# Optimization experiments

Hardware: AMD Instinct MI355X
Metric: run time of the kernel (lower is better)

## Reference

```python
import jax, jax.numpy as jnp
import numpy as np

B, M, C, S, SD, K, H = 32, 448, 384, 512, 128, 8, 8
DH = C // H
EPS = 1e-5
NEG_SLOPE = 0.2


def setup_inputs() -> dict:
    key = jax.random.key(0)
    ks = iter(jax.random.split(key, 32))
    nrm = lambda shape, scale=0.05: (jax.random.normal(next(ks), shape, jnp.float32) * scale)
    inp = {
        'q': jax.random.normal(next(ks), (B, M, C), jnp.float32),
        'coarse': jax.random.normal(next(ks), (B, M, 3), jnp.float32),
        'skeleton': jax.random.normal(next(ks), (B, S, 3), jnp.float32),
        # GraphConv 1: 3 -> 64 (root weight, rel/neighbor weight, bias)
        'gc1_wroot': nrm((3, 64), 0.3), 'gc1_wrel': nrm((3, 64), 0.3), 'gc1_b': jnp.zeros((64,), jnp.float32),
        # GraphConv 2: 64 -> SD
        'gc2_wroot': nrm((64, SD), 0.1), 'gc2_wrel': nrm((64, SD), 0.1), 'gc2_b': jnp.zeros((SD,), jnp.float32),
        # skeleton_projection: SD -> C
        'proj_w': nrm((SD, C), 0.08), 'proj_b': jnp.zeros((C,), jnp.float32),
        # MultiheadAttention (torch layout: in_proj (3C, C), out_proj (C, C))
        'attn_in_w': nrm((3 * C, C), 0.05), 'attn_in_b': jnp.zeros((3 * C,), jnp.float32),
        'attn_out_w': nrm((C, C), 0.05), 'attn_out_b': jnp.zeros((C,), jnp.float32),
        # increase_dim: Conv1d(C,1024,1) + BN(1024) + LeakyReLU + Conv1d(1024,1024,1)
        'inc1_w': nrm((1024, C), 0.05), 'inc1_b': jnp.zeros((1024,), jnp.float32),
        'bn_g': jnp.ones((1024,), jnp.float32), 'bn_b': jnp.zeros((1024,), jnp.float32),
        'bn_m': jnp.zeros((1024,), jnp.float32), 'bn_v': jnp.ones((1024,), jnp.float32),
        'inc2_w': nrm((1024, 1024), 0.03), 'inc2_b': jnp.zeros((1024,), jnp.float32),
        # reduce_map: Linear(C + 1024 + 3, C)
        'red_w': nrm((1024 + C + 3, C), 0.03), 'red_b': jnp.zeros((C,), jnp.float32),
    }
    return inp


def _knn_idx(pts):
    # pts: [B,S,3]; per-batch kNN (self excluded), matching knn_graph(k=K, batch=...)
    d2 = jnp.sum((pts[:, :, None, :] - pts[:, None, :, :]) ** 2, axis=-1)  # [B,S,S]
    d2 = d2 + jnp.eye(S, dtype=pts.dtype)[None] * 1e10                       # mask self
    _, idx = jax.lax.top_k(-d2, K)                                           # [B,S,K]
    return idx


def _graph_conv(x, idx, wroot, wrel, b):
    # GraphConv (PyG, aggr='add'): out_i = x_i Wroot + (sum_{j in N(i)} x_j) Wrel + b
    nb = jax.vmap(lambda f, i: f[i])(x, idx)   # [B,S,K,F]
    agg = nb.sum(axis=2)                       # [B,S,F]
    return x @ wroot + agg @ wrel + b


def reference(q, coarse, skeleton, gc1_wroot, gc1_wrel, gc1_b, gc2_wroot, gc2_wrel, gc2_b,
              proj_w, proj_b, attn_in_w, attn_in_b, attn_out_w, attn_out_b,
              inc1_w, inc1_b, bn_g, bn_b, bn_m, bn_v, inc2_w, inc2_b, red_w, red_b):
    # --- skeleton branch: knn graph + 2-layer GraphConv + max-pool + projection ---
    idx = _knn_idx(skeleton)
    h = _graph_conv(skeleton, idx, gc1_wroot, gc1_wrel, gc1_b)
    h = jax.nn.relu(h)
    h = _graph_conv(h, idx, gc2_wroot, gc2_wrel, gc2_b)        # [B,S,SD]
    proxy = jnp.max(h, axis=1)                                  # [B,SD]
    proxy = proxy @ proj_w + proj_b                             # [B,C]
    kv = jnp.broadcast_to(proxy[:, None, :], (B, M, C))         # expanded proxies

    # --- cross attention (torch nn.MultiheadAttention math) ---
    wq, wk, wv = attn_in_w[:C], attn_in_w[C:2 * C], attn_in_w[2 * C:]
    bq, bk, bv = attn_in_b[:C], attn_in_b[C:2 * C], attn_in_b[2 * C:]
    qh = (q @ wq.T + bq).reshape(B, M, H, DH)
    kh = (kv @ wk.T + bk).reshape(B, M, H, DH)
    vh = (kv @ wv.T + bv).reshape(B, M, H, DH)
    scores = jnp.einsum('bmhd,bnhd->bhmn', qh, kh) / jnp.sqrt(jnp.float32(DH))
    attn = jax.nn.softmax(scores, axis=-1)
    ctx = jnp.einsum('bhmn,bnhd->bmhd', attn, vh).reshape(B, M, C)
    q = ctx @ attn_out_w.T + attn_out_b                         # fused features [B,M,C]

    # --- increase_dim (1x1 conv == matmul) + BN(eval) + LeakyReLU + 1x1 conv ---
    g = jnp.einsum('bmc,oc->bmo', q, inc1_w) + inc1_b           # [B,M,1024]
    g = bn_g * (g - bn_m) * jax.lax.rsqrt(bn_v + EPS) + bn_b
    g = jnp.where(g >= 0, g, NEG_SLOPE * g)
    g = jnp.einsum('bmc,oc->bmo', g, inc2_w) + inc2_b
    global_feature = jnp.max(g, axis=1)                         # [B,1024]

    # --- concat + reduce_map ---
    rebuild = jnp.concatenate([jnp.broadcast_to(global_feature[:, None, :], (B, M, 1024)), q, coarse], axis=-1)
    out = rebuild @ red_w + red_b                               # [B,M,C]
    return out
```

## Files before the change

kernel.cpp:

```cpp
#include <hip/hip_runtime.h>

#define NB 32
#define MM 448
#define CC 384
#define SS 512
#define KNN 8

#define WS_IDX   0u
#define WS_H1    524288u
#define WS_PMAX  (WS_H1 + 4194304u)
#define WS_Q     (WS_PMAX + 262144u)
#define WS_Y     (WS_Q + 49152u)
#define WS_G2    (WS_Y + 131072u)
#define WS_BASEP (WS_G2 + 131072u)
#define WS_PP    WS_H1
#define WS_KV    WS_IDX
#define WS_VV    (WS_IDX + 49152u)

__device__ __forceinline__ float wave_sum(float v) {
#pragma unroll
  for (int m = 1; m < 64; m <<= 1) v += __shfl_xor(v, m, 64);
  return v;
}

__global__ __launch_bounds__(256) void k_knn_gc1(
    const float* __restrict__ skel,
    const float* __restrict__ w1root, const float* __restrict__ w1rel,
    const float* __restrict__ b1,
    int* __restrict__ idx_ws, float* __restrict__ h1_ws)
{
  int b   = blockIdx.x >> 7;
  int grp = blockIdx.x & 127;
  __shared__ __align__(16) float4 sk[SS];
  const float* sb = skel + b * SS * 3;
  for (int t = threadIdx.x; t < SS; t += 256)
    sk[t] = make_float4(sb[t*3+0], sb[t*3+1], sb[t*3+2], 0.f);
  __syncthreads();

  int wave = threadIdx.x >> 6, lane = threadIdx.x & 63;
  int i = grp * 4 + wave;
  float4 pi = sk[i];

  float bd[KNN];
#pragma unroll
  for (int t = 0; t < KNN; t++) {
    int j = lane + (t << 6);
    float4 p = sk[j];
    float d2;
    {
#pragma clang fp contract(off)
      float dx = pi.x - p.x, dy = pi.y - p.y, dz = pi.z - p.z;
      d2 = (dx*dx + dy*dy) + dz*dz;
    }
    bd[t] = (j == i) ? 3e38f : d2;
  }

  int win[KNN];
  int* idx_base = idx_ws + (size_t)(b*SS + i) * KNN;
#pragma unroll
  for (int t = 0; t < KNN; t++) {
    float bestd = bd[0]; int bests = 0;
#pragma unroll
    for (int s = 1; s < KNN; s++)
      if (bd[s] < bestd) { bestd = bd[s]; bests = s; }
    int bestj = lane + (bests << 6);
#pragma unroll
    for (int m = 1; m < 64; m <<= 1) {
      float od = __shfl_xor(bestd, m, 64);
      int   oj = __shfl_xor(bestj, m, 64);
      if (od < bestd || (od == bestd && oj < bestj)) { bestd = od; bestj = oj; }
    }
    win[t] = bestj;
    if (lane == t) idx_base[t] = bestj;
    if ((bestj & 63) == lane) {
      int sl = bestj >> 6;
#pragma unroll
      for (int s = 0; s < KNN; s++) if (s == sl) bd[s] = 3e38f;
    }
  }

  float a0 = 0.f, a1 = 0.f, a2 = 0.f;
#pragma unroll
  for (int t = 0; t < KNN; t++) {
    float4 n = sk[win[t]];
    a0 += n.x; a1 += n.y; a2 += n.z;
  }

  int c = lane;
  float h = b1[c] + pi.x*w1root[c] + pi.y*w1root[64+c] + pi.z*w1root[128+c]
                  + a0*w1rel[c]   + a1*w1rel[64+c]   + a2*w1rel[128+c];
  h = fmaxf(h, 0.f);
  h1_ws[(size_t)(b*SS + i) * 64 + lane] = h;
}

__global__ __launch_bounds__(256) void k_gc2_max(
    const float* __restrict__ h1_ws, const int* __restrict__ idx_ws,
    const float* __restrict__ w2root, const float* __restrict__ w2rel,
    const float* __restrict__ b2, float* __restrict__ pmax)
{
  int b = blockIdx.x >> 4, chunk = blockIdx.x & 15;
  int r0 = chunk * 32;
  __shared__ __align__(16) float X[32*129];
  __shared__ __align__(16) float Wt[32*128];
  __shared__ float mred[8*128];
  __shared__ int nbs[32*KNN];

  const float* h1b = h1_ws + (size_t)b * SS * 64;
  nbs[threadIdx.x] = idx_ws[(b*SS + r0)*KNN + threadIdx.x];
#pragma unroll
  for (int p = 0; p < 8; p++) {
    int idx = threadIdx.x + 256*p;
    int r = idx >> 6, k = idx & 63;
    X[r*129 + k] = h1b[(r0 + r)*64 + k];
  }
  __syncthreads();
#pragma unroll
  for (int p = 0; p < 8; p++) {
    int idx = threadIdx.x + 256*p;
    int r = idx >> 6, k = idx & 63;
    const int* nb = nbs + r*KNN;
    float s = 0.f;
#pragma unroll
    for (int j = 0; j < KNN; j++) s += h1b[nb[j]*64 + k];
    X[r*129 + 64 + k] = s;
  }

  int rg = threadIdx.x >> 5, cg = threadIdx.x & 31;
  float acc[4][4];
#pragma unroll
  for (int r = 0; r < 4; r++)
#pragma unroll
    for (int u = 0; u < 4; u++) acc[r][u] = 0.f;

  const float* wsrc[4] = { w2root, w2root + 32*128, w2rel, w2rel + 32*128 };
#pragma unroll 1
  for (int ch = 0; ch < 4; ch++) {
    __syncthreads();
    const float* ws = wsrc[ch];
#pragma unroll
    for (int p = 0; p < 16; p++) {
      int idx = threadIdx.x + 256*p;
      Wt[idx] = ws[idx];
    }
    __syncthreads();
    int kb = ch * 32;
    const float* xr0 = X + (rg*4+0)*129 + kb;
    const float* xr1 = X + (rg*4+1)*129 + kb;
    const float* xr2 = X + (rg*4+2)*129 + kb;
    const float* xr3 = X + (rg*4+3)*129 + kb;
#pragma unroll 4
    for (int k = 0; k < 32; k++) {
      float4 w4 = *(const float4*)(Wt + k*128 + cg*4);
      float x0 = xr0[k], x1 = xr1[k], x2 = xr2[k], x3 = xr3[k];
      acc[0][0] += x0*w4.x; acc[0][1] += x0*w4.y; acc[0][2] += x0*w4.z; acc[0][3] += x0*w4.w;
      acc[1][0] += x1*w4.x; acc[1][1] += x1*w4.y; acc[1][2] += x1*w4.z; acc[1][3] += x1*w4.w;
      acc[2][0] += x2*w4.x; acc[2][1] += x2*w4.y; acc[2][2] += x2*w4.z; acc[2][3] += x2*w4.w;
      acc[3][0] += x3*w4.x; acc[3][1] += x3*w4.y; acc[3][2] += x3*w4.z; acc[3][3] += x3*w4.w;
    }
  }
#pragma unroll
  for (int u = 0; u < 4; u++)
    mred[rg*128 + cg*4 + u] =
      fmaxf(fmaxf(acc[0][u], acc[1][u]), fmaxf(acc[2][u], acc[3][u]));
  __syncthreads();
  if (threadIdx.x < 128) {
    int col = threadIdx.x;
    float mx = mred[col];
#pragma unroll
    for (int g = 1; g < 8; g++) mx = fmaxf(mx, mred[g*128 + col]);
    pmax[(size_t)(b*16 + chunk)*128 + col] = mx + b2[col];
  }
}

__global__ __launch_bounds__(384) void k_proxy_kv(
    const float* __restrict__ pmax,
    const float* __restrict__ proj_w, const float* __restrict__ proj_b,
    float* __restrict__ kv_ws)
{
  int b = blockIdx.x, t = threadIdx.x;
  __shared__ float proxy[128];
  if (t < 128) {
    float m = -3e38f;
    for (int ch = 0; ch < 16; ch++) m = fmaxf(m, pmax[(size_t)(b*16 + ch)*128 + t]);
    proxy[t] = m;
  }
  __syncthreads();
  float acc = proj_b[t];
  for (int s = 0; s < 128; s++) acc += proxy[s] * proj_w[s*CC + t];
  kv_ws[b*CC + t] = acc;
}

__global__ __launch_bounds__(256) void k_mv384(
    const float* __restrict__ xin, const float* __restrict__ w, int row0,
    const float* __restrict__ bias, int bias0, float* __restrict__ out)
{
  int b = blockIdx.x, og = blockIdx.y;
  int wv = threadIdx.x >> 6, lane = threadIdx.x & 63;
  __shared__ float xs[CC];
  for (int t = threadIdx.x; t < CC; t += 256) xs[t] = xin[b*CC + t];
  __syncthreads();
  float x0 = xs[lane*6+0], x1 = xs[lane*6+1], x2 = xs[lane*6+2];
  float x3 = xs[lane*6+3], x4 = xs[lane*6+4], x5 = xs[lane*6+5];
#pragma unroll
  for (int u = 0; u < 8; u++) {
    int o = og*32 + wv*8 + u;
    const float* wr = w + (size_t)(row0 + o) * CC + lane*6;
    float2 wa = *(const float2*)wr;
    float2 wb = *(const float2*)(wr + 2);
    float2 wc = *(const float2*)(wr + 4);
    float p = wa.x*x0 + wa.y*x1 + wb.x*x2 + wb.y*x3 + wc.x*x4 + wc.y*x5;
    p = wave_sum(p);
    if (lane == 0) out[b*CC + o] = bias[bias0 + o] + p;
  }
}

__global__ __launch_bounds__(256) void k_inc1_bn(
    const float* __restrict__ q_ws, const float* __restrict__ inc1_w,
    const float* __restrict__ inc1_b,
    const float* __restrict__ bng, const float* __restrict__ bnb,
    const float* __restrict__ bnm, const float* __restrict__ bnv,
    float* __restrict__ y_ws)
{
  int b = blockIdx.x >> 4, og = blockIdx.x & 15;
  int t = threadIdx.x;
  int o = og*64 + (t >> 2), qq = t & 3;
  __shared__ __align__(16) float xs[CC];
  for (int i = t; i < CC; i += 256) xs[i] = q_ws[b*CC + i];
  __syncthreads();
  const float* wr = inc1_w + (size_t)o * CC + qq*96;
  const float* xr = xs + qq*96;
  float acc = 0.f;
#pragma unroll
  for (int kk = 0; kk < 96; kk += 4) {
    float4 w4 = *(const float4*)(wr + kk);
    float4 x4 = *(const float4*)(xr + kk);
    acc += w4.x*x4.x + w4.y*x4.y + w4.z*x4.z + w4.w*x4.w;
  }
  acc += __shfl_xor(acc, 1, 64);
  acc += __shfl_xor(acc, 2, 64);
  if (qq == 0) {
    float a = acc + inc1_b[o];
    float z = bng[o] * (a - bnm[o]) * rsqrtf(bnv[o] + 1e-5f) + bnb[o];
    y_ws[b*1024 + o] = (z >= 0.f) ? z : 0.2f * z;
  }
}

__global__ __launch_bounds__(256) void k_inc2(
    const float* __restrict__ y_ws, const float* __restrict__ inc2_w,
    const float* __restrict__ inc2_b, float* __restrict__ g2_ws)
{
  int b = blockIdx.x >> 4, og = blockIdx.x & 15;
  int t = threadIdx.x;
  int o = og*64 + (t >> 2), qq = t & 3;
  __shared__ __align__(16) float xs[1024];
  for (int i = t; i < 1024; i += 256) xs[i] = y_ws[b*1024 + i];
  __syncthreads();
  const float* wr = inc2_w + (size_t)o * 1024 + qq*256;
  const float* xr = xs + qq*256;
  float acc = 0.f;
#pragma unroll 8
  for (int kk = 0; kk < 256; kk += 4) {
    float4 w4 = *(const float4*)(wr + kk);
    float4 x4 = *(const float4*)(xr + kk);
    acc += w4.x*x4.x + w4.y*x4.y + w4.z*x4.z + w4.w*x4.w;
  }
  acc += __shfl_xor(acc, 1, 64);
  acc += __shfl_xor(acc, 2, 64);
  if (qq == 0) g2_ws[b*1024 + o] = acc + inc2_b[o];
}

__global__ __launch_bounds__(256) void k_basep(
    const float* __restrict__ g2_ws, const float* __restrict__ q_ws,
    const float* __restrict__ red_w, float* __restrict__ pp)
{
  int cg = blockIdx.x;
  int o0 = blockIdx.y * 64;
  int c0 = cg * 32;
  __shared__ __align__(16) float xs[32*33];
  __shared__ __align__(16) float wt[32*64];
#pragma unroll
  for (int p = 0; p < 8; p++) {
    int idx = threadIdx.x + 256*p;
    int c = idx >> 6, o = idx & 63;
    wt[idx] = red_w[(size_t)(c0 + c)*CC + o0 + o];
  }
  {
    int b = threadIdx.x >> 3, cp = threadIdx.x & 7;
    const float* src = (cg < 32) ? (g2_ws + b*1024 + c0)
                                 : (q_ws  + b*CC   + (c0 - 1024));
    float4 v = *(const float4*)(src + cp*4);
    xs[(cp*4+0)*33 + b] = v.x;
    xs[(cp*4+1)*33 + b] = v.y;
    xs[(cp*4+2)*33 + b] = v.z;
    xs[(cp*4+3)*33 + b] = v.w;
  }
  __syncthreads();
  int b = threadIdx.x >> 3, og = threadIdx.x & 7;
  float acc[8];
#pragma unroll
  for (int u = 0; u < 8; u++) acc[u] = 0.f;
#pragma unroll 8
  for (int c = 0; c < 32; c++) {
    float xv = xs[c*33 + b];
    float4 w0 = *(const float4*)(wt + c*64 + og*8);
    float4 w1 = *(const float4*)(wt + c*64 + og*8 + 4);
    acc[0] += xv*w0.x; acc[1] += xv*w0.y; acc[2] += xv*w0.z; acc[3] += xv*w0.w;
    acc[4] += xv*w1.x; acc[5] += xv*w1.y; acc[6] += xv*w1.z; acc[7] += xv*w1.w;
  }
  float* dst = pp + (size_t)(cg*32 + b)*CC + o0 + og*8;
  *(float4*)dst       = make_float4(acc[0], acc[1], acc[2], acc[3]);
  *(float4*)(dst + 4) = make_float4(acc[4], acc[5], acc[6], acc[7]);
}

__global__ __launch_bounds__(256) void k_base_red(
    const float* __restrict__ pp, float* __restrict__ basep)
{
  int idx = blockIdx.x * 256 + threadIdx.x;
  float s = 0.f;
#pragma unroll 4
  for (int cg = 0; cg < 44; cg++) s += pp[cg*12288 + idx];
  basep[idx] = s;
}

__global__ __launch_bounds__(256) void k_out(
    const float* __restrict__ basep, const float* __restrict__ red_b,
    const float* __restrict__ red_w, const float* __restrict__ coarse,
    float* __restrict__ out)
{
  int gid = blockIdx.x * 256 + threadIdx.x;
  int c4 = gid % 96;
  int row = gid / 96;
  int b = row / 448;
  int c = c4 * 4;
  float4 p0 = *(const float4*)(basep + b*CC + c);
  float4 rb = *(const float4*)(red_b + c);
  const float* cr = coarse + (size_t)row * 3;
  float cx = cr[0], cy = cr[1], cz = cr[2];
  float4 w0 = *(const float4*)(red_w + (size_t)1408*CC + c);
  float4 w1 = *(const float4*)(red_w + (size_t)1409*CC + c);
  float4 w2 = *(const float4*)(red_w + (size_t)1410*CC + c);
  float4 o4;
  o4.x = p0.x + rb.x + cx*w0.x + cy*w1.x + cz*w2.x;
  o4.y = p0.y + rb.y + cx*w0.y + cy*w1.y + cz*w2.y;
  o4.z = p0.z + rb.z + cx*w0.z + cy*w1.z + cz*w2.z;
  o4.w = p0.w + rb.w + cx*w0.w + cy*w1.w + cz*w2.w;
  *(float4*)(out + (size_t)row*CC + c) = o4;
}

extern "C" void kernel_launch(void* const* d_in, const int* in_sizes, int n_in,
                              void* d_out, int out_size, void* d_ws, size_t ws_size,
                              hipStream_t stream)
{
  (void)in_sizes; (void)n_in; (void)out_size; (void)ws_size;
  const float* coarse = (const float*)d_in[1];
  const float* skel   = (const float*)d_in[2];
  const float* g1wr   = (const float*)d_in[3];
  const float* g1wl   = (const float*)d_in[4];
  const float* g1b    = (const float*)d_in[5];
  const float* g2wr   = (const float*)d_in[6];
  const float* g2wl   = (const float*)d_in[7];
  const float* g2b    = (const float*)d_in[8];
  const float* projw  = (const float*)d_in[9];
  const float* projb  = (const float*)d_in[10];
  const float* aiw    = (const float*)d_in[11];
  const float* aib    = (const float*)d_in[12];
  const float* aow    = (const float*)d_in[13];
  const float* aob    = (const float*)d_in[14];
  const float* i1w    = (const float*)d_in[15];
  const float* i1b    = (const float*)d_in[16];
  const float* bng    = (const float*)d_in[17];
  const float* bnb    = (const float*)d_in[18];
  const float* bnm    = (const float*)d_in[19];
  const float* bnv    = (const float*)d_in[20];
  const float* i2w    = (const float*)d_in[21];
  const float* i2b    = (const float*)d_in[22];
  const float* redw   = (const float*)d_in[23];
  const float* redb   = (const float*)d_in[24];
  float* out = (float*)d_out;

  char* ws = (char*)d_ws;
  int*   idx_ws = (int*)(ws + WS_IDX);
  float* h1_ws  = (float*)(ws + WS_H1);
  float* pmax   = (float*)(ws + WS_PMAX);
  float* q_ws   = (float*)(ws + WS_Q);
  float* y_ws   = (float*)(ws + WS_Y);
  float* g2_ws  = (float*)(ws + WS_G2);
  float* basep  = (float*)(ws + WS_BASEP);
  float* pp     = (float*)(ws + WS_PP);
  float* kv_ws  = (float*)(ws + WS_KV);
  float* vv_ws  = (float*)(ws + WS_VV);

  k_knn_gc1<<<4096, 256, 0, stream>>>(skel, g1wr, g1wl, g1b, idx_ws, h1_ws);
  k_gc2_max<<<512, 256, 0, stream>>>(h1_ws, idx_ws, g2wr, g2wl, g2b, pmax);
  k_proxy_kv<<<32, 384, 0, stream>>>(pmax, projw, projb, kv_ws);
  k_mv384<<<dim3(32, 12), 256, 0, stream>>>(kv_ws, aiw, 2*CC, aib, 2*CC, vv_ws);
  k_mv384<<<dim3(32, 12), 256, 0, stream>>>(vv_ws, aow, 0,    aob, 0,    q_ws);
  k_inc1_bn<<<512, 256, 0, stream>>>(q_ws, i1w, i1b, bng, bnb, bnm, bnv, y_ws);
  k_inc2<<<512, 256, 0, stream>>>(y_ws, i2w, i2b, g2_ws);
  k_basep<<<dim3(44, 6), 256, 0, stream>>>(g2_ws, q_ws, redw, pp);
  k_base_red<<<48, 256, 0, stream>>>(pp, basep);
  k_out<<<5376, 256, 0, stream>>>(basep, redb, redw, coarse, out);
}
```

Baseline: 234.2 us.

## Fuse proxy/attention/inc1 matvec chain into one kernel and simplify reduce-map base

Merges the proxy projection, V projection, out-projection and inc1+BN+LeakyReLU into a single per-batch kernel (4 blocks per batch). Each block recomputes the shared small matvecs redundantly so that it can produce its own 256-output slice of inc1. The reduce_map base term is now one kernel per (batch, 64-col group) with in-block reduction, which removes the partial-product buffer and the separate reduction kernel. The goal is to drop four kernel launches and their intermediate global round trips. In exchange the fused kernel has low parallelism (128 blocks) and does serial per-thread 384-length dot products with strided, uncoalesced weight reads.

Result: slower. 284.2 us (+21.4%).

```diff
diff --git a/kernel.cpp b/kernel.cpp
--- a/kernel.cpp
+++ b/kernel.cpp
@@ -13,15 +13,6 @@
 #define WS_Y     (WS_Q + 49152u)
 #define WS_G2    (WS_Y + 131072u)
 #define WS_BASEP (WS_G2 + 131072u)
-#define WS_PP    WS_H1
-#define WS_KV    WS_IDX
-#define WS_VV    (WS_IDX + 49152u)
-
-__device__ __forceinline__ float wave_sum(float v) {
-#pragma unroll
-  for (int m = 1; m < 64; m <<= 1) v += __shfl_xor(v, m, 64);
-  return v;
-}
 
 __global__ __launch_bounds__(256) void k_knn_gc1(
     const float* __restrict__ skel,
@@ -172,75 +163,72 @@
   }
 }
 
-__global__ __launch_bounds__(384) void k_proxy_kv(
+__global__ __launch_bounds__(256) void k_mid(
     const float* __restrict__ pmax,
     const float* __restrict__ proj_w, const float* __restrict__ proj_b,
-    float* __restrict__ kv_ws)
-{
-  int b = blockIdx.x, t = threadIdx.x;
-  __shared__ float proxy[128];
+    const float* __restrict__ aiw, const float* __restrict__ aib,
+    const float* __restrict__ aow, const float* __restrict__ aob,
+    const float* __restrict__ i1w, const float* __restrict__ i1b,
+    const float* __restrict__ bng, const float* __restrict__ bnb,
+    const float* __restrict__ bnm, const float* __restrict__ bnv,
+    float* __restrict__ q_ws, float* __restrict__ y_ws)
+{
+  int b = blockIdx.x >> 2, sl = blockIdx.x & 3;
+  int t = threadIdx.x;
+  __shared__ __align__(16) float proxy[128];
+  __shared__ __align__(16) float kv[CC];
+  __shared__ __align__(16) float vv[CC];
+  __shared__ __align__(16) float qv[CC];
+
   if (t < 128) {
     float m = -3e38f;
-    for (int ch = 0; ch < 16; ch++) m = fmaxf(m, pmax[(size_t)(b*16 + ch)*128 + t]);
+    for (int ch = 0; ch < 16; ch++)
+      m = fmaxf(m, pmax[(size_t)(b*16 + ch)*128 + t]);
     proxy[t] = m;
   }
   __syncthreads();
-  float acc = proj_b[t];
-  for (int s = 0; s < 128; s++) acc += proxy[s] * proj_w[s*CC + t];
-  kv_ws[b*CC + t] = acc;
-}
-
-__global__ __launch_bounds__(256) void k_mv384(
-    const float* __restrict__ xin, const float* __restrict__ w, int row0,
-    const float* __restrict__ bias, int bias0, float* __restrict__ out)
-{
-  int b = blockIdx.x, og = blockIdx.y;
-  int wv = threadIdx.x >> 6, lane = threadIdx.x & 63;
-  __shared__ float xs[CC];
-  for (int t = threadIdx.x; t < CC; t += 256) xs[t] = xin[b*CC + t];
-  __syncthreads();
-  float x0 = xs[lane*6+0], x1 = xs[lane*6+1], x2 = xs[lane*6+2];
-  float x3 = xs[lane*6+3], x4 = xs[lane*6+4], x5 = xs[lane*6+5];
-#pragma unroll
-  for (int u = 0; u < 8; u++) {
-    int o = og*32 + wv*8 + u;
-    const float* wr = w + (size_t)(row0 + o) * CC + lane*6;
-    float2 wa = *(const float2*)wr;
-    float2 wb = *(const float2*)(wr + 2);
-    float2 wc = *(const float2*)(wr + 4);
-    float p = wa.x*x0 + wa.y*x1 + wb.x*x2 + wb.y*x3 + wc.x*x4 + wc.y*x5;
-    p = wave_sum(p);
-    if (lane == 0) out[b*CC + o] = bias[bias0 + o] + p;
-  }
-}
-
-__global__ __launch_bounds__(256) void k_inc1_bn(
-    const float* __restrict__ q_ws, const float* __restrict__ inc1_w,
-    const float* __restrict__ inc1_b,
-    const float* __restrict__ bng, const float* __restrict__ bnb,
-    const float* __restrict__ bnm, const float* __restrict__ bnv,
-    float* __restrict__ y_ws)
-{
-  int b = blockIdx.x >> 4, og = blockIdx.x & 15;
-  int t = threadIdx.x;
-  int o = og*64 + (t >> 2), qq = t & 3;
-  __shared__ __align__(16) float xs[CC];
-  for (int i = t; i < CC; i += 256) xs[i] = q_ws[b*CC + i];
-  __syncthreads();
-  const float* wr = inc1_w + (size_t)o * CC + qq*96;
-  const float* xr = xs + qq*96;
-  float acc = 0.f;
-#pragma unroll
-  for (int kk = 0; kk < 96; kk += 4) {
-    float4 w4 = *(const float4*)(wr + kk);
-    float4 x4 = *(const float4*)(xr + kk);
-    acc += w4.x*x4.x + w4.y*x4.y + w4.z*x4.z + w4.w*x4.w;
-  }
-  acc += __shfl_xor(acc, 1, 64);
-  acc += __shfl_xor(acc, 2, 64);
-  if (qq == 0) {
-    float a = acc + inc1_b[o];
-    float z = bng[o] * (a - bnm[o]) * rsqrtf(bnv[o] + 1e-5f) + bnb[o];
+  for (int c = t; c < CC; c += 256) {
+    float acc = proj_b[c];
+    for (int s = 0; s < 128; s++) acc += proxy[s] * proj_w[s*CC + c];
+    kv[c] = acc;
+  }
+  __syncthreads();
+  for (int o = t; o < CC; o += 256) {
+    const float* wr = aiw + (size_t)(2*CC + o) * CC;
+    float acc = aib[2*CC + o];
+#pragma unroll 8
+    for (int k = 0; k < CC; k += 4) {
+      float4 w4 = *(const float4*)(wr + k);
+      float4 x4 = *(const float4*)(kv + k);
+      acc += w4.x*x4.x + w4.y*x4.y + w4.z*x4.z + w4.w*x4.w;
+    }
+    vv[o] = acc;
+  }
+  __syncthreads();
+  for (int o = t; o < CC; o += 256) {
+    const float* wr = aow + (size_t)o * CC;
+    float acc = aob[o];
+#pragma unroll 8
+    for (int k = 0; k < CC; k += 4) {
+      float4 w4 = *(const float4*)(wr + k);
+      float4 x4 = *(const float4*)(vv + k);
+      acc += w4.x*x4.x + w4.y*x4.y + w4.z*x4.z + w4.w*x4.w;
+    }
+    qv[o] = acc;
+    if (sl == 0) q_ws[b*CC + o] = acc;
+  }
+  __syncthreads();
+  {
+    int o = sl*256 + t;
+    const float* wr = i1w + (size_t)o * CC;
+    float acc = i1b[o];
+#pragma unroll 8
+    for (int k = 0; k < CC; k += 4) {
+      float4 w4 = *(const float4*)(wr + k);
+      float4 x4 = *(const float4*)(qv + k);
+      acc += w4.x*x4.x + w4.y*x4.y + w4.z*x4.z + w4.w*x4.w;
+    }
+    float z = bng[o] * (acc - bnm[o]) * rsqrtf(bnv[o] + 1e-5f) + bnb[o];
     y_ws[b*1024 + o] = (z >= 0.f) ? z : 0.2f * z;
   }
 }
@@ -269,57 +257,32 @@
   if (qq == 0) g2_ws[b*1024 + o] = acc + inc2_b[o];
 }
 
-__global__ __launch_bounds__(256) void k_basep(
+__global__ __launch_bounds__(256) void k_base(
     const float* __restrict__ g2_ws, const float* __restrict__ q_ws,
-    const float* __restrict__ red_w, float* __restrict__ pp)
-{
-  int cg = blockIdx.x;
-  int o0 = blockIdx.y * 64;
-  int c0 = cg * 32;
-  __shared__ __align__(16) float xs[32*33];
-  __shared__ __align__(16) float wt[32*64];
-#pragma unroll
-  for (int p = 0; p < 8; p++) {
-    int idx = threadIdx.x + 256*p;
-    int c = idx >> 6, o = idx & 63;
-    wt[idx] = red_w[(size_t)(c0 + c)*CC + o0 + o];
-  }
-  {
-    int b = threadIdx.x >> 3, cp = threadIdx.x & 7;
-    const float* src = (cg < 32) ? (g2_ws + b*1024 + c0)
-                                 : (q_ws  + b*CC   + (c0 - 1024));
-    float4 v = *(const float4*)(src + cp*4);
-    xs[(cp*4+0)*33 + b] = v.x;
-    xs[(cp*4+1)*33 + b] = v.y;
-    xs[(cp*4+2)*33 + b] = v.z;
-    xs[(cp*4+3)*33 + b] = v.w;
-  }
-  __syncthreads();
-  int b = threadIdx.x >> 3, og = threadIdx.x & 7;
-  float acc[8];
-#pragma unroll
-  for (int u = 0; u < 8; u++) acc[u] = 0.f;
-#pragma unroll 8
-  for (int c = 0; c < 32; c++) {
-    float xv = xs[c*33 + b];
-    float4 w0 = *(const float4*)(wt + c*64 + og*8);
-    float4 w1 = *(const float4*)(wt + c*64 + og*8 + 4);
-    acc[0] += xv*w0.x; acc[1] += xv*w0.y; acc[2] += xv*w0.z; acc[3] += xv*w0.w;
-    acc[4] += xv*w1.x; acc[5] += xv*w1.y; acc[6] += xv*w1.z; acc[7] += xv*w1.w;
-  }
-  float* dst = pp + (size_t)(cg*32 + b)*CC + o0 + og*8;
-  *(float4*)dst       = make_float4(acc[0], acc[1], acc[2], acc[3]);
-  *(float4*)(dst + 4) = make_float4(acc[4], acc[5], acc[6], acc[7]);
-}
-
-__global__ __launch_bounds__(256) void k_base_red(
-    const float* __restrict__ pp, float* __restrict__ basep)
-{
-  int idx = blockIdx.x * 256 + threadIdx.x;
-  float s = 0.f;
+    const float* __restrict__ red_w, float* __restrict__ basep)
+{
+  int b = blockIdx.x >> 3;
+  int o0 = (blockIdx.x & 7) * 64;
+  b = blockIdx.x;
+  o0 = blockIdx.y * 64;
+  int wv = threadIdx.x >> 6, lane = threadIdx.x & 63;
+  __shared__ __align__(16) float X[1408];
+  __shared__ float part[4][64];
+  for (int i = threadIdx.x; i < 1408; i += 256)
+    X[i] = (i < 1024) ? g2_ws[b*1024 + i] : q_ws[b*CC + (i - 1024)];
+  __syncthreads();
+  int k0 = wv * 352;
+  float acc = 0.f;
+  const float* wbase = red_w + o0 + lane;
 #pragma unroll 4
-  for (int cg = 0; cg < 44; cg++) s += pp[cg*12288 + idx];
-  basep[idx] = s;
+  for (int k = 0; k < 352; k++)
+    acc += X[k0 + k] * wbase[(size_t)(k0 + k) * CC];
+  part[wv][lane] = acc;
+  __syncthreads();
+  if (threadIdx.x < 64) {
+    float s = part[0][lane] + part[1][lane] + part[2][lane] + part[3][lane];
+    basep[b*CC + o0 + lane] = s;
+  }
 }
 
 __global__ __launch_bounds__(256) void k_out(
@@ -386,18 +349,12 @@
   float* y_ws   = (float*)(ws + WS_Y);
   float* g2_ws  = (float*)(ws + WS_G2);
   float* basep  = (float*)(ws + WS_BASEP);
-  float* pp     = (float*)(ws + WS_PP);
-  float* kv_ws  = (float*)(ws + WS_KV);
-  float* vv_ws  = (float*)(ws + WS_VV);
 
   k_knn_gc1<<<4096, 256, 0, stream>>>(skel, g1wr, g1wl, g1b, idx_ws, h1_ws);
   k_gc2_max<<<512, 256, 0, stream>>>(h1_ws, idx_ws, g2wr, g2wl, g2b, pmax);
-  k_proxy_kv<<<32, 384, 0, stream>>>(pmax, projw, projb, kv_ws);
-  k_mv384<<<dim3(32, 12), 256, 0, stream>>>(kv_ws, aiw, 2*CC, aib, 2*CC, vv_ws);
-  k_mv384<<<dim3(32, 12), 256, 0, stream>>>(vv_ws, aow, 0,    aob, 0,    q_ws);
-  k_inc1_bn<<<512, 256, 0, stream>>>(q_ws, i1w, i1b, bng, bnb, bnm, bnv, y_ws);
+  k_mid<<<128, 256, 0, stream>>>(pmax, projw, projb, aiw, aib, aow, aob,
+                                 i1w, i1b, bng, bnb, bnm, bnv, q_ws, y_ws);
   k_inc2<<<512, 256, 0, stream>>>(y_ws, i2w, i2b, g2_ws);
-  k_basep<<<dim3(44, 6), 256, 0, stream>>>(g2_ws, q_ws, redw, pp);
-  k_base_red<<<48, 256, 0, stream>>>(pp, basep);
+  k_base<<<dim3(32, 6), 256, 0, stream>>>(g2_ws, q_ws, redw, basep);
   k_out<<<5376, 256, 0, stream>>>(basep, redb, redw, coarse, out);
 }
```
